# Kernel optimization log

Measured on AMD Instinct MI355X. Metric: run time of the kernel, lower is better.

Reference implementation:

```python
import jax, jax.numpy as jnp
import numpy as np

B, INPUT_DIM, EMB_DIM = 16384, 2048, 768
DOMAIN_NUM, MEMORY_NUM, TAU = 9, 10, 32.0


def setup_inputs() -> dict:
    key = jax.random.key(0)
    k1, k2, k3, k4, k5 = jax.random.split(key, 5)
    feature = jax.random.normal(k1, (B, INPUT_DIM), dtype=jnp.float32)
    category = jax.random.randint(k2, (B,), 0, DOMAIN_NUM, dtype=jnp.int64)
    # Linear(input_dim, emb_dim, bias=False) weights: [emb_dim, input_dim]
    W_topic = jax.random.normal(k3, (EMB_DIM, INPUT_DIM), dtype=jnp.float32) * 0.02
    W_domain = jax.random.normal(k4, (EMB_DIM, INPUT_DIM), dtype=jnp.float32) * 0.02
    # domain_num Embedding(memory_num, emb_dim) tables, stacked: [D, M, E]
    memory_tables = jax.random.normal(k5, (DOMAIN_NUM, MEMORY_NUM, EMB_DIM), dtype=jnp.float32)
    return {"feature": feature, "W_topic": W_topic, "W_domain": W_domain,
            "memory_tables": memory_tables, "category": category}


def reference(feature, W_topic, W_domain, memory_tables, category):
    eps = 1e-12
    # F.normalize(feature, p=2, dim=-1)
    norm = jnp.maximum(jnp.linalg.norm(feature, axis=-1, keepdims=True), eps)
    feat = feature / norm                                   # [B, I]
    # per-sample gather of each sample's category memory table: [B, M, E]
    mem = memory_tables[category]
    # faithful quirk: loop over domain_num indexes the BATCH dim of the stack
    D = memory_tables.shape[0]
    mems_d = mem[:D]                                        # [D, M, E]
    t = feat @ W_topic.T                                    # [B, E]
    topic_att = jax.nn.softmax(jnp.einsum('be,dme->bdm', t, mems_d) * TAU, axis=-1)
    sep = jnp.einsum('bdm,dme->bde', topic_att, mems_d)     # [B, D, E]
    dproj = feat @ W_domain.T                               # [B, E]
    domain_att = jax.nn.softmax(jnp.einsum('bde,be->bd', sep, dproj) * TAU, axis=-1)
    return domain_att[:, None, :]                           # [B, 1, D]
```

## Files before the change

### kernel.cpp

```cpp
#include <hip/hip_runtime.h>
#include <math.h>

#define TAU_F 32.0f

typedef __attribute__((ext_vector_type(8))) _Float16 half8;
typedef __attribute__((ext_vector_type(4))) float f32x4;

union HU { uint4 u; half8 v; };

__global__ __launch_bounds__(256) void gproj2(
    const float* __restrict__ Wt, const float* __restrict__ Wd,
    const float* __restrict__ mem, const int* __restrict__ cat,
    float* __restrict__ P)
{
    __shared__ float Ml[96 * 36];
    __shared__ float Wl[32 * 68];

    const int bid = blockIdx.x;
    const int mat = bid >> 7;
    const int ks  = (bid >> 5) & 3;
    const int ct  = bid & 31;
    const int c0  = ct * 64;
    const int tid = threadIdx.x;
    const float* __restrict__ W = mat ? Wd : Wt;

    const int tr = tid >> 4;
    const int tc = tid & 15;

    float acc[6][4];
    #pragma unroll
    for (int j = 0; j < 6; ++j)
        #pragma unroll
        for (int q = 0; q < 4; ++q) acc[j][q] = 0.f;

    for (int ch = 0; ch < 6; ++ch) {
        __syncthreads();
        #pragma unroll
        for (int p = 0; p < 3; ++p) {
            const int idx = tid + 256 * p;
            const int r   = idx >> 3;
            const int kq  = idx & 7;
            float4 v = make_float4(0.f, 0.f, 0.f, 0.f);
            if (r < 90) {
                const int d = r / 10;
                const int mrow = cat[d] * 10 + (r - d * 10);
                v = *(const float4*)(mem + (size_t)mrow * 768 + ks * 192 + ch * 32 + kq * 4);
            }
            *(float4*)(Ml + r * 36 + kq * 4) = v;
        }
        #pragma unroll
        for (int p = 0; p < 2; ++p) {
            const int idx = tid + 256 * p;
            const int e   = idx >> 4;
            const int c4  = (idx & 15) * 4;
            *(float4*)(Wl + e * 68 + c4) =
                *(const float4*)(W + (size_t)(ks * 192 + ch * 32 + e) * 2048 + c0 + c4);
        }
        __syncthreads();

        #pragma unroll
        for (int e = 0; e < 32; e += 4) {
            float4 m4[6], w4[4];
            #pragma unroll
            for (int j = 0; j < 6; ++j) m4[j] = *(const float4*)(Ml + (tr * 6 + j) * 36 + e);
            #pragma unroll
            for (int q = 0; q < 4; ++q) w4[q] = *(const float4*)(Wl + (e + q) * 68 + tc * 4);
            #pragma unroll
            for (int j = 0; j < 6; ++j) {
                const float mv[4] = {m4[j].x, m4[j].y, m4[j].z, m4[j].w};
                #pragma unroll
                for (int q = 0; q < 4; ++q) {
                    acc[j][0] = fmaf(mv[q], w4[q].x, acc[j][0]);
                    acc[j][1] = fmaf(mv[q], w4[q].y, acc[j][1]);
                    acc[j][2] = fmaf(mv[q], w4[q].z, acc[j][2]);
                    acc[j][3] = fmaf(mv[q], w4[q].w, acc[j][3]);
                }
            }
        }
    }

    #pragma unroll
    for (int j = 0; j < 6; ++j) {
        float4 v = make_float4(acc[j][0], acc[j][1], acc[j][2], acc[j][3]);
        *(float4*)(P + (size_t)ks * 192 * 2048 + (size_t)(mat * 96 + tr * 6 + j) * 2048 + c0 + tc * 4) = v;
    }
}

__global__ __launch_bounds__(256) void split_g2(
    const float* __restrict__ P,
    unsigned short* __restrict__ gH2, unsigned short* __restrict__ gL2)
{
    const int u  = blockIdx.x * 256 + threadIdx.x;
    const int n  = u >> 8;
    const int k0 = (u & 255) * 8;

    float s[8] = {0.f, 0.f, 0.f, 0.f, 0.f, 0.f, 0.f, 0.f};
    #pragma unroll
    for (int ks = 0; ks < 4; ++ks) {
        const float4 a = *(const float4*)(P + (size_t)ks * 393216 + (size_t)n * 2048 + k0);
        const float4 b = *(const float4*)(P + (size_t)ks * 393216 + (size_t)n * 2048 + k0 + 4);
        s[0] += a.x; s[1] += a.y; s[2] += a.z; s[3] += a.w;
        s[4] += b.x; s[5] += b.y; s[6] += b.z; s[7] += b.w;
    }
    union { _Float16 h[8]; uint4 u4; } hi, lo;
    #pragma unroll
    for (int e = 0; e < 8; ++e) {
        const _Float16 h = (_Float16)s[e];
        hi.h[e] = h;
        lo.h[e] = (_Float16)(s[e] - (float)h);
    }
    const int kc = k0 >> 5, lq = (k0 >> 3) & 3;
    const size_t dst = ((size_t)(kc * 4 + lq) * 192 + n) * 8;
    *(uint4*)(gH2 + dst) = hi.u4;
    *(uint4*)(gL2 + dst) = lo.u4;
}

#define SPAD 201

__global__ __launch_bounds__(512, 2) void fused_mfma2(
    const float* __restrict__ feat,
    const unsigned short* __restrict__ gH2, const unsigned short* __restrict__ gL2,
    float* __restrict__ out)
{
    __shared__ float scores[64 * SPAD];
    __shared__ float ssqp[2][64];

    const int tid  = threadIdx.x;
    const int row0 = blockIdx.x * 64;
    const int w  = tid >> 6, l = tid & 63;
    const int lm = l & 15,  lq = l >> 4;
    const int kw = w & 1,   nq = w >> 1;

    f32x4 acc[4][3];
    #pragma unroll
    for (int i = 0; i < 4; ++i)
        #pragma unroll
        for (int j = 0; j < 3; ++j) acc[i][j] = (f32x4)0.f;
    float ssq[4] = {0.f, 0.f, 0.f, 0.f};

    const float* aB[4];
    #pragma unroll
    for (int i = 0; i < 4; ++i)
        aB[i] = feat + (size_t)(row0 + i * 16 + lm) * 2048 + lq * 8;
    const int bbase = (nq * 48 + lm) * 8 + lq * 1536;

    float4 ar[4][2]; uint4 bh[3], bl[3];
    #pragma unroll
    for (int i = 0; i < 4; ++i) {
        ar[i][0] = *(const float4*)(aB[i] + kw * 32);
        ar[i][1] = *(const float4*)(aB[i] + kw * 32 + 4);
    }
    #pragma unroll
    for (int j = 0; j < 3; ++j) {
        const int off = bbase + kw * 6144 + j * 128;
        bh[j] = *(const uint4*)(gH2 + off);
        bl[j] = *(const uint4*)(gL2 + off);
    }

    for (int kc = kw; kc < 64; kc += 2) {
        half8 fh[4], fl[4];
        #pragma unroll
        for (int i = 0; i < 4; ++i) {
            const float xs[8] = {ar[i][0].x, ar[i][0].y, ar[i][0].z, ar[i][0].w,
                                 ar[i][1].x, ar[i][1].y, ar[i][1].z, ar[i][1].w};
            union { _Float16 h[8]; half8 v; } uh, ul;
            #pragma unroll
            for (int e = 0; e < 8; ++e) {
                const float x = xs[e];
                const _Float16 h = (_Float16)x;
                uh.h[e] = h;
                ul.h[e] = (_Float16)(x - (float)h);
                if (nq == 0) ssq[i] = fmaf(x, x, ssq[i]);
            }
            fh[i] = uh.v; fl[i] = ul.v;
        }
        const int kn = (kc + 2 < 64) ? kc + 2 : kw;
        float4 arn[4][2]; uint4 bhn[3], bln[3];
        #pragma unroll
        for (int i = 0; i < 4; ++i) {
            arn[i][0] = *(const float4*)(aB[i] + kn * 32);
            arn[i][1] = *(const float4*)(aB[i] + kn * 32 + 4);
        }
        #pragma unroll
        for (int j = 0; j < 3; ++j) {
            const int off = bbase + kn * 6144 + j * 128;
            bhn[j] = *(const uint4*)(gH2 + off);
            bln[j] = *(const uint4*)(gL2 + off);
        }
        #pragma unroll
        for (int j = 0; j < 3; ++j) {
            HU h8, l8; h8.u = bh[j]; l8.u = bl[j];
            #pragma unroll
            for (int i = 0; i < 4; ++i) {
                acc[i][j] = __builtin_amdgcn_mfma_f32_16x16x32_f16(fh[i], h8.v, acc[i][j], 0, 0, 0);
                acc[i][j] = __builtin_amdgcn_mfma_f32_16x16x32_f16(fh[i], l8.v, acc[i][j], 0, 0, 0);
                acc[i][j] = __builtin_amdgcn_mfma_f32_16x16x32_f16(fl[i], h8.v, acc[i][j], 0, 0, 0);
            }
        }
        #pragma unroll
        for (int i = 0; i < 4; ++i) { ar[i][0] = arn[i][0]; ar[i][1] = arn[i][1]; }
        #pragma unroll
        for (int j = 0; j < 3; ++j) { bh[j] = bhn[j]; bl[j] = bln[j]; }
    }

    if (nq == 0) {
        #pragma unroll
        for (int i = 0; i < 4; ++i) {
            ssq[i] += __shfl_xor(ssq[i], 16, 64);
            ssq[i] += __shfl_xor(ssq[i], 32, 64);
        }
        if (l < 16)
            #pragma unroll
            for (int i = 0; i < 4; ++i) ssqp[kw][i * 16 + lm] = ssq[i];
    }

    if (kw == 0) {
        #pragma unroll
        for (int i = 0; i < 4; ++i)
            #pragma unroll
            for (int j = 0; j < 3; ++j)
                #pragma unroll
                for (int r = 0; r < 4; ++r)
                    scores[(i * 16 + lq * 4 + r) * SPAD + nq * 48 + j * 16 + lm] = acc[i][j][r];
    }
    __syncthreads();
    if (kw == 1) {
        #pragma unroll
        for (int i = 0; i < 4; ++i)
            #pragma unroll
            for (int j = 0; j < 3; ++j)
                #pragma unroll
                for (int r = 0; r < 4; ++r)
                    scores[(i * 16 + lq * 4 + r) * SPAD + nq * 48 + j * 16 + lm] += acc[i][j][r];
    }
    __syncthreads();

    if (tid < 64) {
        const int r = tid;
        const float nsq = ssqp[0][r] + ssqp[1][r];
        const float inv = TAU_F / fmaxf(sqrtf(nsq), 1e-12f);
        const float* sc = scores + r * SPAD;
        float lg[9];
        float dmax = -1e30f;
        #pragma unroll
        for (int d = 0; d < 9; ++d) {
            const float* v = sc + d * 10;
            const float* u = sc + 96 + d * 10;
            float mx = v[0];
            #pragma unroll
            for (int m = 1; m < 10; ++m) mx = fmaxf(mx, v[m]);
            float s = 0.f, dot = 0.f;
            #pragma unroll
            for (int m = 0; m < 10; ++m) {
                const float p = __expf((v[m] - mx) * inv);
                s += p;
                dot = fmaf(p, u[m], dot);
            }
            const float lgt = (dot / s) * inv;
            lg[d] = lgt;
            dmax = fmaxf(dmax, lgt);
        }
        float s2 = 0.f;
        #pragma unroll
        for (int d = 0; d < 9; ++d) { const float p = __expf(lg[d] - dmax); lg[d] = p; s2 += p; }
        const float r2 = 1.0f / s2;
        #pragma unroll
        for (int d = 0; d < 9; ++d)
            out[(size_t)(row0 + r) * 9 + d] = lg[d] * r2;
    }
}

extern "C" void kernel_launch(void* const* d_in, const int* in_sizes, int n_in,
                              void* d_out, int out_size, void* d_ws, size_t ws_size,
                              hipStream_t stream) {
    const float* feature = (const float*)d_in[0];
    const float* Wt      = (const float*)d_in[1];
    const float* Wd      = (const float*)d_in[2];
    const float* mem     = (const float*)d_in[3];
    const int*   cat     = (const int*)d_in[4];

    float* P = (float*)d_ws;
    unsigned short* gH2 = (unsigned short*)((char*)d_ws + (size_t)4 * 192 * 2048 * 4);
    unsigned short* gL2 = gH2 + (size_t)192 * 2048;
    float* out = (float*)d_out;

    gproj2<<<256, 256, 0, stream>>>(Wt, Wd, mem, cat, P);
    split_g2<<<192, 256, 0, stream>>>(P, gH2, gL2);
    fused_mfma2<<<256, 512, 0, stream>>>(feature, gH2, gL2, out);
}
```

Measured before the change: 287.6 us.

## Stage split fp16 feature tiles in LDS and use fragment-ordered weight layout

```diff
diff --git a/kernel.cpp b/kernel.cpp
--- a/kernel.cpp
+++ b/kernel.cpp
@@ -7,6 +7,7 @@
 typedef __attribute__((ext_vector_type(4))) float f32x4;
 
 union HU { uint4 u; half8 v; };
+union H4 { _Float16 h[4]; uint2 u2; };
 
 __global__ __launch_bounds__(256) void gproj2(
     const float* __restrict__ Wt, const float* __restrict__ Wd,
@@ -82,13 +83,12 @@
     #pragma unroll
     for (int j = 0; j < 6; ++j) {
         float4 v = make_float4(acc[j][0], acc[j][1], acc[j][2], acc[j][3]);
-        *(float4*)(P + (size_t)ks * 192 * 2048 + (size_t)(mat * 96 + tr * 6 + j) * 2048 + c0 + tc * 4) = v;
-    }
-}
-
-__global__ __launch_bounds__(256) void split_g2(
-    const float* __restrict__ P,
-    unsigned short* __restrict__ gH2, unsigned short* __restrict__ gL2)
+        *(float4*)(P + (size_t)ks * 393216 + (size_t)(mat * 96 + tr * 6 + j) * 2048 + c0 + tc * 4) = v;
+    }
+}
+
+__global__ __launch_bounds__(256) void split_g3(
+    const float* __restrict__ P, unsigned short* __restrict__ gB)
 {
     const int u  = blockIdx.x * 256 + threadIdx.x;
     const int n  = u >> 8;
@@ -109,137 +109,145 @@
         hi.h[e] = h;
         lo.h[e] = (_Float16)(s[e] - (float)h);
     }
-    const int kc = k0 >> 5, lq = (k0 >> 3) & 3;
-    const size_t dst = ((size_t)(kc * 4 + lq) * 192 + n) * 8;
-    *(uint4*)(gH2 + dst) = hi.u4;
-    *(uint4*)(gL2 + dst) = lo.u4;
-}
-
-#define SPAD 201
-
-__global__ __launch_bounds__(512, 2) void fused_mfma2(
-    const float* __restrict__ feat,
-    const unsigned short* __restrict__ gH2, const unsigned short* __restrict__ gL2,
+    const int kc = k0 >> 5;
+    const int lq = (k0 >> 3) & 3;
+    const int nq = n / 48;
+    const int rm = n - nq * 48;
+    const int j  = rm >> 4;
+    const int lm = rm & 15;
+    const size_t fH = (size_t)((kc * 12 + nq * 3 + j) * 2 + 0) * 512 + lq * 128 + lm * 8;
+    const size_t fL = (size_t)((kc * 12 + nq * 3 + j) * 2 + 1) * 512 + lq * 128 + lm * 8;
+    *(uint4*)(gB + fH) = hi.u4;
+    *(uint4*)(gB + fL) = lo.u4;
+}
+
+#define SPAD 196
+
+__global__ __launch_bounds__(256, 2) void fused_mfma3(
+    const float* __restrict__ feat, const unsigned short* __restrict__ gB,
     float* __restrict__ out)
 {
-    __shared__ float scores[64 * SPAD];
-    __shared__ float ssqp[2][64];
+    __shared__ __align__(16) char smem[25088];
+    __shared__ float ssqf[32];
+    unsigned short* aS = (unsigned short*)smem;
+    float* scores = (float*)smem;
 
     const int tid  = threadIdx.x;
-    const int row0 = blockIdx.x * 64;
-    const int w  = tid >> 6, l = tid & 63;
+    const int row0 = blockIdx.x * 32;
+    const int nq = tid >> 6, l = tid & 63;
     const int lm = l & 15,  lq = l >> 4;
-    const int kw = w & 1,   nq = w >> 1;
-
-    f32x4 acc[4][3];
-    #pragma unroll
-    for (int i = 0; i < 4; ++i)
+
+    const int srow = tid >> 3;
+    const int skq  = tid & 7;
+
+    f32x4 acc[2][3];
+    #pragma unroll
+    for (int i = 0; i < 2; ++i)
         #pragma unroll
         for (int j = 0; j < 3; ++j) acc[i][j] = (f32x4)0.f;
-    float ssq[4] = {0.f, 0.f, 0.f, 0.f};
-
-    const float* aB[4];
-    #pragma unroll
-    for (int i = 0; i < 4; ++i)
-        aB[i] = feat + (size_t)(row0 + i * 16 + lm) * 2048 + lq * 8;
-    const int bbase = (nq * 48 + lm) * 8 + lq * 1536;
-
-    float4 ar[4][2]; uint4 bh[3], bl[3];
-    #pragma unroll
-    for (int i = 0; i < 4; ++i) {
-        ar[i][0] = *(const float4*)(aB[i] + kw * 32);
-        ar[i][1] = *(const float4*)(aB[i] + kw * 32 + 4);
-    }
+    float ssq = 0.f;
+
+    const float* fptr = feat + (size_t)(row0 + srow) * 2048 + skq * 4;
+
+    const unsigned short* bptr = gB + (size_t)(nq * 3) * 2 * 512 + l * 8;
+
+    float4 fA  = *(const float4*)(fptr);
+    float4 fd1 = *(const float4*)(fptr + 32);
+    float4 fd2 = *(const float4*)(fptr + 64);
+    uint4 bh[3], bl[3];
     #pragma unroll
     for (int j = 0; j < 3; ++j) {
-        const int off = bbase + kw * 6144 + j * 128;
-        bh[j] = *(const uint4*)(gH2 + off);
-        bl[j] = *(const uint4*)(gL2 + off);
-    }
-
-    for (int kc = kw; kc < 64; kc += 2) {
-        half8 fh[4], fl[4];
-        #pragma unroll
-        for (int i = 0; i < 4; ++i) {
-            const float xs[8] = {ar[i][0].x, ar[i][0].y, ar[i][0].z, ar[i][0].w,
-                                 ar[i][1].x, ar[i][1].y, ar[i][1].z, ar[i][1].w};
-            union { _Float16 h[8]; half8 v; } uh, ul;
-            #pragma unroll
-            for (int e = 0; e < 8; ++e) {
+        bh[j] = *(const uint4*)(bptr + j * 1024);
+        bl[j] = *(const uint4*)(bptr + j * 1024 + 512);
+    }
+    {
+        const float xs[4] = {fA.x, fA.y, fA.z, fA.w};
+        H4 h, lo;
+        #pragma unroll
+        for (int e = 0; e < 4; ++e) {
+            const float x = xs[e];
+            ssq = fmaf(x, x, ssq);
+            const _Float16 hh = (_Float16)x;
+            h.h[e]  = hh;
+            lo.h[e] = (_Float16)(x - (float)hh);
+        }
+        *(uint2*)(aS + (size_t)(0 * 32 + srow) * 40 + skq * 4) = h.u2;
+        *(uint2*)(aS + (size_t)(1 * 32 + srow) * 40 + skq * 4) = lo.u2;
+    }
+    __syncthreads();
+
+    for (int kc = 0; kc < 64; ++kc) {
+        const int kf = (kc + 3 < 64) ? kc + 3 : 63;
+        float4 fd3 = *(const float4*)(fptr + kf * 32);
+        const int kb = (kc + 1 < 64) ? kc + 1 : 63;
+        uint4 bhn[3], bln[3];
+        #pragma unroll
+        for (int j = 0; j < 3; ++j) {
+            bhn[j] = *(const uint4*)(bptr + (size_t)kb * 12288 + j * 1024);
+            bln[j] = *(const uint4*)(bptr + (size_t)kb * 12288 + j * 1024 + 512);
+        }
+
+        if (kc < 63) {
+            const int nb = (kc + 1) & 1;
+            const float xs[4] = {fd1.x, fd1.y, fd1.z, fd1.w};
+            H4 h, lo;
+            #pragma unroll
+            for (int e = 0; e < 4; ++e) {
                 const float x = xs[e];
-                const _Float16 h = (_Float16)x;
-                uh.h[e] = h;
-                ul.h[e] = (_Float16)(x - (float)h);
-                if (nq == 0) ssq[i] = fmaf(x, x, ssq[i]);
-            }
-            fh[i] = uh.v; fl[i] = ul.v;
-        }
-        const int kn = (kc + 2 < 64) ? kc + 2 : kw;
-        float4 arn[4][2]; uint4 bhn[3], bln[3];
-        #pragma unroll
-        for (int i = 0; i < 4; ++i) {
-            arn[i][0] = *(const float4*)(aB[i] + kn * 32);
-            arn[i][1] = *(const float4*)(aB[i] + kn * 32 + 4);
-        }
-        #pragma unroll
-        for (int j = 0; j < 3; ++j) {
-            const int off = bbase + kn * 6144 + j * 128;
-            bhn[j] = *(const uint4*)(gH2 + off);
-            bln[j] = *(const uint4*)(gL2 + off);
-        }
+                ssq = fmaf(x, x, ssq);
+                const _Float16 hh = (_Float16)x;
+                h.h[e]  = hh;
+                lo.h[e] = (_Float16)(x - (float)hh);
+            }
+            *(uint2*)(aS + (size_t)((nb * 2 + 0) * 32 + srow) * 40 + skq * 4) = h.u2;
+            *(uint2*)(aS + (size_t)((nb * 2 + 1) * 32 + srow) * 40 + skq * 4) = lo.u2;
+        }
+
+        const int cb = kc & 1;
+        half8 fh[2], fl[2];
+        #pragma unroll
+        for (int i = 0; i < 2; ++i) {
+            HU t0, t1;
+            t0.u = *(const uint4*)(aS + (size_t)((cb * 2 + 0) * 32 + i * 16 + lm) * 40 + lq * 8);
+            t1.u = *(const uint4*)(aS + (size_t)((cb * 2 + 1) * 32 + i * 16 + lm) * 40 + lq * 8);
+            fh[i] = t0.v; fl[i] = t1.v;
+        }
+
         #pragma unroll
         for (int j = 0; j < 3; ++j) {
             HU h8, l8; h8.u = bh[j]; l8.u = bl[j];
             #pragma unroll
-            for (int i = 0; i < 4; ++i) {
+            for (int i = 0; i < 2; ++i) {
                 acc[i][j] = __builtin_amdgcn_mfma_f32_16x16x32_f16(fh[i], h8.v, acc[i][j], 0, 0, 0);
                 acc[i][j] = __builtin_amdgcn_mfma_f32_16x16x32_f16(fh[i], l8.v, acc[i][j], 0, 0, 0);
                 acc[i][j] = __builtin_amdgcn_mfma_f32_16x16x32_f16(fl[i], h8.v, acc[i][j], 0, 0, 0);
             }
         }
-        #pragma unroll
-        for (int i = 0; i < 4; ++i) { ar[i][0] = arn[i][0]; ar[i][1] = arn[i][1]; }
+        __syncthreads();
+
+        fd1 = fd2; fd2 = fd3;
         #pragma unroll
         for (int j = 0; j < 3; ++j) { bh[j] = bhn[j]; bl[j] = bln[j]; }
     }
 
-    if (nq == 0) {
-        #pragma unroll
-        for (int i = 0; i < 4; ++i) {
-            ssq[i] += __shfl_xor(ssq[i], 16, 64);
-            ssq[i] += __shfl_xor(ssq[i], 32, 64);
-        }
-        if (l < 16)
-            #pragma unroll
-            for (int i = 0; i < 4; ++i) ssqp[kw][i * 16 + lm] = ssq[i];
-    }
-
-    if (kw == 0) {
-        #pragma unroll
-        for (int i = 0; i < 4; ++i)
-            #pragma unroll
-            for (int j = 0; j < 3; ++j)
-                #pragma unroll
-                for (int r = 0; r < 4; ++r)
-                    scores[(i * 16 + lq * 4 + r) * SPAD + nq * 48 + j * 16 + lm] = acc[i][j][r];
-    }
+    ssq += __shfl_xor(ssq, 1, 64);
+    ssq += __shfl_xor(ssq, 2, 64);
+    ssq += __shfl_xor(ssq, 4, 64);
+    if ((tid & 7) == 0) ssqf[tid >> 3] = ssq;
+
+    #pragma unroll
+    for (int i = 0; i < 2; ++i)
+        #pragma unroll
+        for (int j = 0; j < 3; ++j)
+            #pragma unroll
+            for (int r = 0; r < 4; ++r)
+                scores[(size_t)(i * 16 + lq * 4 + r) * SPAD + nq * 48 + j * 16 + lm] = acc[i][j][r];
     __syncthreads();
-    if (kw == 1) {
-        #pragma unroll
-        for (int i = 0; i < 4; ++i)
-            #pragma unroll
-            for (int j = 0; j < 3; ++j)
-                #pragma unroll
-                for (int r = 0; r < 4; ++r)
-                    scores[(i * 16 + lq * 4 + r) * SPAD + nq * 48 + j * 16 + lm] += acc[i][j][r];
-    }
-    __syncthreads();
-
-    if (tid < 64) {
+
+    if (tid < 32) {
         const int r = tid;
-        const float nsq = ssqp[0][r] + ssqp[1][r];
-        const float inv = TAU_F / fmaxf(sqrtf(nsq), 1e-12f);
-        const float* sc = scores + r * SPAD;
+        const float inv = TAU_F / fmaxf(sqrtf(ssqf[r]), 1e-12f);
+        const float* sc = scores + (size_t)r * SPAD;
         float lg[9];
         float dmax = -1e30f;
         #pragma unroll
@@ -280,11 +288,10 @@
     const int*   cat     = (const int*)d_in[4];
 
     float* P = (float*)d_ws;
-    unsigned short* gH2 = (unsigned short*)((char*)d_ws + (size_t)4 * 192 * 2048 * 4);
-    unsigned short* gL2 = gH2 + (size_t)192 * 2048;
+    unsigned short* gB = (unsigned short*)((char*)d_ws + (size_t)4 * 192 * 2048 * 4);
     float* out = (float*)d_out;
 
     gproj2<<<256, 256, 0, stream>>>(Wt, Wd, mem, cat, P);
-    split_g2<<<192, 256, 0, stream>>>(P, gH2, gL2);
-    fused_mfma2<<<256, 512, 0, stream>>>(feature, gH2, gL2, out);
-}
+    split_g3<<<192, 256, 0, stream>>>(P, gB);
+    fused_mfma3<<<512, 256, 0, stream>>>(feature, gB, out);
+}
```

Result: faster. 268.2 us (-6.7%).
